# Kernel tuning notes

Measured on AMD Instinct MI355X. Metric: run time of the kernel, lower is better.

## Reference

```python
import jax, jax.numpy as jnp
import numpy as np

BETA = 0.95
SG_SLOPE = 25.0

@jax.custom_vjp
def spike(mem, thr):
    return (mem > thr).astype(mem.dtype)

def _spike_fwd(mem, thr):
    return spike(mem, thr), (mem, thr)

def _spike_bwd(res, g):
    mem, thr = res
    s = jax.nn.sigmoid(SG_SLOPE * (mem - thr))
    return (g * (SG_SLOPE * s * (1.0 - s)), jnp.zeros_like(thr))

spike.defvjp(_spike_fwd, _spike_bwd)

def setup_inputs() -> dict:
    key = jax.random.key(0)
    ks = jax.random.split(key, 7)
    T, B, IN, H, OUT = 50, 512, 784, 800, 10
    return {
        "x":  jax.random.normal(ks[0], (T, B, IN), dtype=jnp.float32),
        "W1": jax.random.normal(ks[1], (H, IN), dtype=jnp.float32) / np.sqrt(IN),
        "b1": jax.random.normal(ks[2], (H,), dtype=jnp.float32) * 0.01,
        "W2": jax.random.normal(ks[3], (H, H), dtype=jnp.float32) / np.sqrt(H),
        "b2": jax.random.normal(ks[4], (H,), dtype=jnp.float32) * 0.01,
        "W3": jax.random.normal(ks[5], (OUT, H), dtype=jnp.float32) / np.sqrt(H),
        "b3": jax.random.normal(ks[6], (OUT,), dtype=jnp.float32) * 0.01,
        "thresh1": jnp.ones((H,), dtype=jnp.float32),
        "thresh2": jnp.ones((H,), dtype=jnp.float32),
    }

def reference(x, W1, b1, W2, b2, W3, b3, thresh1, thresh2):
    T, B = x.shape[0], x.shape[1]
    H, OUT = W1.shape[0], W3.shape[0]
    # Batch the input projection across all timesteps: [T,B,H]
    x1 = jnp.einsum('tbi,hi->tbh', x, W1) + b1

    def step(carry, xt):
        mem1, mem2, mem3 = carry
        mem1 = BETA * mem1 + xt
        spk1 = spike(mem1, thresh1)
        mem1 = mem1 * (1.0 - spk1)
        mem2 = BETA * mem2 + spk1 @ W2.T + b2
        spk2 = spike(mem2, thresh2)
        mem2 = mem2 * (1.0 - spk2)
        mem3 = BETA * mem3 + spk2 @ W3.T + b3
        spk3 = spike(mem3, jnp.float32(1.0))
        mem3 = mem3 * (1.0 - spk3)
        return (mem1, mem2, mem3), (spk1, spk2, spk3)

    init = (jnp.zeros((B, H), x.dtype), jnp.zeros((B, H), x.dtype), jnp.zeros((B, OUT), x.dtype))
    _, (s1r, s2r, s3r) = jax.lax.scan(step, init, x1)
    return s3r.sum(0), s1r, s2r, s3r
```

## Files before the change

### kernel.cpp

```cpp
#include <hip/hip_runtime.h>

#define TT 50
#define BB 512
#define II 784
#define HH 800
#define OO 10
#define BH (BB*HH)
#define MM (TT*BB)

typedef double d4 __attribute__((ext_vector_type(4)));

__device__ __forceinline__ int dec16(double V) {
    const int vi = (int)(V + 0.5);
    const int a = vi - 96;
    if (a >= 0 && a < 64 && (a & 3) == 0) return a >> 2;
    return ((vi - 6) >> 4) & 15;
}
__device__ __forceinline__ bool isf1(double V) {
    const int vi = (int)(V + 0.5);
    const int a = vi - 96;
    return (a >= 0 && a < 64 && (a & 3) == 0);
}

__global__ __launch_bounds__(256) void k_gemm1(
    const float* __restrict__ x, const float* __restrict__ W1,
    const float* __restrict__ b1, double* __restrict__ x1d)
{
    __shared__ float As[16*144];
    __shared__ float Bs[16*80];
    const int m0 = blockIdx.x * 128;
    const int n0 = blockIdx.y * 80;
    const int tid = threadIdx.x;
    const int lane = tid & 63;
    const int wm = (tid >> 6) * 32;

    const d4 zc = {0.0, 0.0, 0.0, 0.0};
    const d4 pr = __builtin_amdgcn_mfma_f64_16x16x4f64(
        (double)lane, 1.0, zc, 0, 0, 0);
    const d4 pc = __builtin_amdgcn_mfma_f64_16x16x4f64(
        1.0, (double)lane, zc, 0, 0, 0);
    int rowIdx[4], colIdx[4];
    #pragma unroll
    for (int r = 0; r < 4; ++r) {
        rowIdx[r] = dec16(pr[r]) & 15;
        colIdx[r] = dec16(pc[r]) & 15;
    }
    const bool af1 = isf1(pr[0]);
    const bool bf1 = isf1(pc[0]);
    const int arow = af1 ? (lane & 15) : (lane >> 2);
    const int akk  = af1 ? (lane >> 4) : (lane & 3);
    const int bcol = bf1 ? (lane & 15) : (lane >> 2);
    const int bkk  = bf1 ? (lane >> 4) : (lane & 3);

    d4 acc[2][5] = {};

    const int sm = tid >> 1;
    const int sk = (tid & 1) * 8;
    const int bn0 = tid >> 2, bk0 = (tid & 3) * 4;
    const int q1  = tid + 256;
    const int bn1 = q1 >> 2,  bk1 = (q1 & 3) * 4;

    for (int k0 = 0; k0 < II; k0 += 16) {
        const float4 a0 = *(const float4*)(x + (long)(m0+sm)*II + k0 + sk);
        const float4 a1 = *(const float4*)(x + (long)(m0+sm)*II + k0 + sk + 4);
        const float4 w0 = *(const float4*)(W1 + (long)(n0+bn0)*II + k0 + bk0);
        float4 w1;
        if (tid < 64)
            w1 = *(const float4*)(W1 + (long)(n0+bn1)*II + k0 + bk1);
        __syncthreads();
        As[(sk+0)*144+sm] = a0.x;
        As[(sk+1)*144+sm] = a0.y;
        As[(sk+2)*144+sm] = a0.z;
        As[(sk+3)*144+sm] = a0.w;
        As[(sk+4)*144+sm] = a1.x;
        As[(sk+5)*144+sm] = a1.y;
        As[(sk+6)*144+sm] = a1.z;
        As[(sk+7)*144+sm] = a1.w;
        Bs[(bk0+0)*80+bn0] = w0.x;
        Bs[(bk0+1)*80+bn0] = w0.y;
        Bs[(bk0+2)*80+bn0] = w0.z;
        Bs[(bk0+3)*80+bn0] = w0.w;
        if (tid < 64) {
            Bs[(bk1+0)*80+bn1] = w1.x;
            Bs[(bk1+1)*80+bn1] = w1.y;
            Bs[(bk1+2)*80+bn1] = w1.z;
            Bs[(bk1+3)*80+bn1] = w1.w;
        }
        __syncthreads();
        #pragma unroll
        for (int s = 0; s < 4; ++s) {
            const int ka = 4*s + akk;
            const int kb = 4*s + bkk;
            const double a0d = (double)As[ka*144 + wm + arow];
            const double a1d = (double)As[ka*144 + wm + 16 + arow];
            double bd[5];
            #pragma unroll
            for (int j = 0; j < 5; ++j)
                bd[j] = (double)Bs[kb*80 + 16*j + bcol];
            #pragma unroll
            for (int j = 0; j < 5; ++j) {
                acc[0][j] = __builtin_amdgcn_mfma_f64_16x16x4f64(
                    a0d, bd[j], acc[0][j], 0, 0, 0);
                acc[1][j] = __builtin_amdgcn_mfma_f64_16x16x4f64(
                    a1d, bd[j], acc[1][j], 0, 0, 0);
            }
        }
    }
    #pragma unroll
    for (int i = 0; i < 2; ++i) {
        #pragma unroll
        for (int r = 0; r < 4; ++r) {
            const long m = m0 + wm + 16*i + rowIdx[r];
            #pragma unroll
            for (int j = 0; j < 5; ++j) {
                const int n = n0 + 16*j + colIdx[r];
                x1d[m*HH + n] = acc[i][j][r] + (double)b1[n];
            }
        }
    }
}

__global__ __launch_bounds__(256) void k_mem1(
    const double* __restrict__ x1d, const float* __restrict__ thresh1,
    unsigned char* __restrict__ s1c, float* __restrict__ s1r)
{
    const int lid = blockIdx.x*256 + threadIdx.x;
    const int h = lid % HH;
    const double th = (double)thresh1[h];
    double mem = 0.0;
    for (int t = 0; t < TT; ++t) {
        const long idx = (long)t*BH + lid;
        mem = 0.95*mem + x1d[idx];
        const bool spk = mem > th;
        s1c[idx] = spk ? 1 : 0;
        s1r[idx] = spk ? 1.0f : 0.0f;
        if (spk) mem = 0.0;
    }
}

__global__ __launch_bounds__(256) void k_gemm2(
    const unsigned char* __restrict__ s1c, const float* __restrict__ W2,
    float* __restrict__ z2)
{
    __shared__ float As[32*132];
    __shared__ float Bs[32*84];
    const int m0 = blockIdx.x * 128;
    const int n0 = blockIdx.y * 80;
    const int tid = threadIdx.x;
    const int tx = tid & 15, ty = tid >> 4;
    float acc[8][5] = {};

    const int sm = tid >> 1;
    const int sk = (tid & 1) * 16;
    const int b0n = tid >> 3,        b0k = (tid & 7) * 4;
    const int q1 = tid + 256, b1n = q1 >> 3, b1k = (q1 & 7) * 4;
    const int q2 = tid + 512, b2n = q2 >> 3, b2k = (q2 & 7) * 4;

    for (int k0 = 0; k0 < HH; k0 += 32) {
        const uint4 av = *(const uint4*)(s1c + (long)(m0+sm)*HH + k0 + sk);
        const float4 w0 = *(const float4*)(W2 + (long)(n0+b0n)*HH + k0 + b0k);
        const float4 w1 = *(const float4*)(W2 + (long)(n0+b1n)*HH + k0 + b1k);
        float4 w2;
        if (tid < 128)
            w2 = *(const float4*)(W2 + (long)(n0+b2n)*HH + k0 + b2k);
        __syncthreads();
        {
            const unsigned int d[4] = {av.x, av.y, av.z, av.w};
            #pragma unroll
            for (int w = 0; w < 4; ++w) {
                #pragma unroll
                for (int j = 0; j < 4; ++j)
                    As[(sk + w*4 + j)*132 + sm] =
                        (float)((d[w] >> (8*j)) & 0xffu);
            }
        }
        Bs[(b0k+0)*84+b0n] = w0.x; Bs[(b0k+1)*84+b0n] = w0.y;
        Bs[(b0k+2)*84+b0n] = w0.z; Bs[(b0k+3)*84+b0n] = w0.w;
        Bs[(b1k+0)*84+b1n] = w1.x; Bs[(b1k+1)*84+b1n] = w1.y;
        Bs[(b1k+2)*84+b1n] = w1.z; Bs[(b1k+3)*84+b1n] = w1.w;
        if (tid < 128) {
            Bs[(b2k+0)*84+b2n] = w2.x; Bs[(b2k+1)*84+b2n] = w2.y;
            Bs[(b2k+2)*84+b2n] = w2.z; Bs[(b2k+3)*84+b2n] = w2.w;
        }
        __syncthreads();
        #pragma unroll
        for (int k = 0; k < 32; ++k) {
            float a[8], b[5];
            #pragma unroll
            for (int i = 0; i < 8; ++i) a[i] = As[k*132 + ty*8 + i];
            #pragma unroll
            for (int j = 0; j < 4; ++j) b[j] = Bs[k*84 + tx*4 + j];
            b[4] = Bs[k*84 + 64 + tx];
            #pragma unroll
            for (int i = 0; i < 8; ++i)
                #pragma unroll
                for (int j = 0; j < 5; ++j)
                    acc[i][j] = __fmaf_rn(a[i], b[j], acc[i][j]);
        }
    }
    #pragma unroll
    for (int i = 0; i < 8; ++i) {
        const long m = m0 + ty*8 + i;
        #pragma unroll
        for (int j = 0; j < 4; ++j)
            z2[m*HH + n0 + tx*4 + j] = acc[i][j];
        z2[m*HH + n0 + 64 + tx] = acc[i][4];
    }
}

__global__ __launch_bounds__(256) void k_scan2(
    const float* __restrict__ z2, const float* __restrict__ b2,
    const float* __restrict__ thresh2, float* __restrict__ s2r,
    unsigned char* __restrict__ s2c)
{
    const int lid = blockIdx.x*256 + threadIdx.x;
    const int n = lid % HH;
    const float b2v = b2[n];
    const float thv = thresh2[n];
    float m = 0.0f;
    for (int t = 0; t < TT; ++t) {
        const long idx = (long)t*BH + lid;
        const float m2 = __fadd_rn(
            __fadd_rn(__fmul_rn(0.95f, m), z2[idx]), b2v);
        const bool spk = m2 > thv;
        s2r[idx] = spk ? 1.0f : 0.0f;
        s2c[idx] = spk ? 1 : 0;
        m = spk ? 0.0f : m2;
    }
}

__global__ __launch_bounds__(256) void k_gemm3(
    const unsigned char* __restrict__ s2c, const float* __restrict__ W3,
    float* __restrict__ z3)
{
    const long m = blockIdx.x*256 + threadIdx.x;
    const unsigned char* row = s2c + m*HH;
    float acc[10] = {};
    for (int k0 = 0; k0 < HH; k0 += 16) {
        const uint4 v = *(const uint4*)(row + k0);
        const unsigned int d[4] = {v.x, v.y, v.z, v.w};
        #pragma unroll
        for (int w = 0; w < 4; ++w) {
            #pragma unroll
            for (int j = 0; j < 4; ++j) {
                const float sv = (float)((d[w] >> (8*j)) & 0xffu);
                const int k = k0 + w*4 + j;
                #pragma unroll
                for (int o = 0; o < 10; ++o)
                    acc[o] = __fmaf_rn(sv, W3[o*HH + k], acc[o]);
            }
        }
    }
    #pragma unroll
    for (int o = 0; o < 10; ++o)
        z3[m*OO + o] = acc[o];
}

__global__ __launch_bounds__(256) void k_scan3(
    const float* __restrict__ z3, const float* __restrict__ b3,
    float* __restrict__ s3r, float* __restrict__ out0)
{
    const int gid = blockIdx.x*256 + threadIdx.x;
    if (gid >= BB*OO) return;
    const int o = gid % OO;
    const float b3v = b3[o];
    float mem = 0.0f, cnt = 0.0f;
    for (int t = 0; t < TT; ++t) {
        const float m3 = __fadd_rn(
            __fadd_rn(__fmul_rn(0.95f, mem), z3[(long)t*BB*OO + gid]), b3v);
        const bool spk = m3 > 1.0f;
        s3r[(long)t*BB*OO + gid] = spk ? 1.0f : 0.0f;
        if (spk) cnt = __fadd_rn(cnt, 1.0f);
        mem = spk ? 0.0f : m3;
    }
    out0[gid] = cnt;
}

extern "C" void kernel_launch(void* const* d_in, const int* in_sizes, int n_in,
                              void* d_out, int out_size, void* d_ws, size_t ws_size,
                              hipStream_t stream)
{
    const float* x   = (const float*)d_in[0];
    const float* W1  = (const float*)d_in[1];
    const float* b1  = (const float*)d_in[2];
    const float* W2  = (const float*)d_in[3];
    const float* b2  = (const float*)d_in[4];
    const float* W3  = (const float*)d_in[5];
    const float* b3  = (const float*)d_in[6];
    const float* th1 = (const float*)d_in[7];
    const float* th2 = (const float*)d_in[8];

    float* out0 = (float*)d_out;
    float* s1r  = out0 + BB*OO;
    float* s2r  = s1r + (long)TT*BH;
    float* s3r  = s2r + (long)TT*BH;

    char* p = (char*)d_ws;
    double* x1d = (double*)p;
    float*  z2  = (float*)p;
    float*  z3  = (float*)(p + 84000000);
    unsigned char* s1c = (unsigned char*)(p + 163840000);
    unsigned char* s2c = s1c + (size_t)TT*BH;
    (void)ws_size;

    k_gemm1<<<dim3(200,10), dim3(256), 0, stream>>>(x, W1, b1, x1d);
    k_mem1 <<<dim3(1600),   dim3(256), 0, stream>>>(x1d, th1, s1c, s1r);
    k_gemm2<<<dim3(200,10), dim3(256), 0, stream>>>(s1c, W2, z2);
    k_scan2<<<dim3(1600),   dim3(256), 0, stream>>>(z2, b2, th2, s2r, s2c);
    k_gemm3<<<dim3(100),    dim3(256), 0, stream>>>(s2c, W3, z3);
    k_scan3<<<dim3(20),     dim3(256), 0, stream>>>(z3, b3, s3r, out0);
}
```

Baseline: 1.406 ms.

## Double-buffer gemm1 shared tiles with register prefetch and deeper K chunks

Rewrites the input-projection GEMM main loop to use double-buffered shared memory with K chunks of 32 instead of 16. Global loads for chunk c+2 are issued into registers while chunk c is computed, and the store for chunk c+1 goes into the alternate buffer, so there is one barrier per chunk instead of two. This is meant to hide global memory latency and cut synchronisation. In exchange it roughly quadruples shared memory per block and raises register pressure, which could lower occupancy.

```diff
diff --git a/kernel.cpp b/kernel.cpp
--- a/kernel.cpp
+++ b/kernel.cpp
@@ -22,12 +22,37 @@
     return (a >= 0 && a < 64 && (a & 3) == 0);
 }
 
+template<int NS>
+__device__ __forceinline__ void gemm1_compute(
+    const float* __restrict__ Ab, const float* __restrict__ Bb,
+    int wm, int arow, int akk, int bcol, int bkk, d4 acc[2][5])
+{
+    #pragma unroll
+    for (int s = 0; s < NS; ++s) {
+        const int ka = 4*s + akk;
+        const int kb = 4*s + bkk;
+        const double a0d = (double)Ab[ka*144 + wm + arow];
+        const double a1d = (double)Ab[ka*144 + wm + 16 + arow];
+        double bd[5];
+        #pragma unroll
+        for (int j = 0; j < 5; ++j)
+            bd[j] = (double)Bb[kb*80 + 16*j + bcol];
+        #pragma unroll
+        for (int j = 0; j < 5; ++j) {
+            acc[0][j] = __builtin_amdgcn_mfma_f64_16x16x4f64(
+                a0d, bd[j], acc[0][j], 0, 0, 0);
+            acc[1][j] = __builtin_amdgcn_mfma_f64_16x16x4f64(
+                a1d, bd[j], acc[1][j], 0, 0, 0);
+        }
+    }
+}
+
 __global__ __launch_bounds__(256) void k_gemm1(
     const float* __restrict__ x, const float* __restrict__ W1,
     const float* __restrict__ b1, double* __restrict__ x1d)
 {
-    __shared__ float As[16*144];
-    __shared__ float Bs[16*80];
+    __shared__ float As[2][32*144];
+    __shared__ float Bs[2][32*80];
     const int m0 = blockIdx.x * 128;
     const int n0 = blockIdx.y * 80;
     const int tid = threadIdx.x;
@@ -54,58 +79,88 @@
 
     d4 acc[2][5] = {};
 
-    const int sm = tid >> 1;
-    const int sk = (tid & 1) * 8;
-    const int bn0 = tid >> 2, bk0 = (tid & 3) * 4;
-    const int q1  = tid + 256;
-    const int bn1 = q1 >> 2,  bk1 = (q1 & 3) * 4;
-
-    for (int k0 = 0; k0 < II; k0 += 16) {
-        const float4 a0 = *(const float4*)(x + (long)(m0+sm)*II + k0 + sk);
-        const float4 a1 = *(const float4*)(x + (long)(m0+sm)*II + k0 + sk + 4);
-        const float4 w0 = *(const float4*)(W1 + (long)(n0+bn0)*II + k0 + bk0);
-        float4 w1;
-        if (tid < 64)
-            w1 = *(const float4*)(W1 + (long)(n0+bn1)*II + k0 + bk1);
+    const int koff = (tid & 7) * 4;
+    const int r0   = tid >> 3;
+    const float* pA0 = x + (long)(m0 + r0      )*II + koff;
+    const float* pA1 = x + (long)(m0 + r0 + 32 )*II + koff;
+    const float* pA2 = x + (long)(m0 + r0 + 64 )*II + koff;
+    const float* pA3 = x + (long)(m0 + r0 + 96 )*II + koff;
+    const float* pB0 = W1 + (long)(n0 + r0     )*II + koff;
+    const float* pB1 = W1 + (long)(n0 + r0 + 32)*II + koff;
+    const int rB2 = (tid < 128) ? (r0 + 64) : 79;
+    const float* pB2 = W1 + (long)(n0 + rB2)*II + koff;
+
+    float4 RA0, RA1, RA2, RA3, RB0, RB1, RB2;
+
+#define G1_LOAD(c) do {                                                  \
+        const int _k0 = 32*(c);                                          \
+        const int _kc = ((c) == 24) ? 16 : 32;                           \
+        if (koff < _kc) {                                                \
+            RA0 = *(const float4*)(pA0 + _k0);                           \
+            RA1 = *(const float4*)(pA1 + _k0);                           \
+            RA2 = *(const float4*)(pA2 + _k0);                           \
+            RA3 = *(const float4*)(pA3 + _k0);                           \
+            RB0 = *(const float4*)(pB0 + _k0);                           \
+            RB1 = *(const float4*)(pB1 + _k0);                           \
+            if (tid < 128) RB2 = *(const float4*)(pB2 + _k0);            \
+        }                                                                \
+    } while (0)
+
+#define G1_STORE(c) do {                                                 \
+        float* _Ad = As[(c) & 1];                                        \
+        float* _Bd = Bs[(c) & 1];                                        \
+        const int _kc = ((c) == 24) ? 16 : 32;                           \
+        if (koff < _kc) {                                                \
+            _Ad[(koff+0)*144 + r0      ] = RA0.x;                        \
+            _Ad[(koff+1)*144 + r0      ] = RA0.y;                        \
+            _Ad[(koff+2)*144 + r0      ] = RA0.z;                        \
+            _Ad[(koff+3)*144 + r0      ] = RA0.w;                        \
+            _Ad[(koff+0)*144 + r0 + 32 ] = RA1.x;                        \
+            _Ad[(koff+1)*144 + r0 + 32 ] = RA1.y;                        \
+            _Ad[(koff+2)*144 + r0 + 32 ] = RA1.z;                        \
+            _Ad[(koff+3)*144 + r0 + 32 ] = RA1.w;                        \
+            _Ad[(koff+0)*144 + r0 + 64 ] = RA2.x;                        \
+            _Ad[(koff+1)*144 + r0 + 64 ] = RA2.y;                        \
+            _Ad[(koff+2)*144 + r0 + 64 ] = RA2.z;                        \
+            _Ad[(koff+3)*144 + r0 + 64 ] = RA2.w;                        \
+            _Ad[(koff+0)*144 + r0 + 96 ] = RA3.x;                        \
+            _Ad[(koff+1)*144 + r0 + 96 ] = RA3.y;                        \
+            _Ad[(koff+2)*144 + r0 + 96 ] = RA3.z;                        \
+            _Ad[(koff+3)*144 + r0 + 96 ] = RA3.w;                        \
+            _Bd[(koff+0)*80 + r0       ] = RB0.x;                        \
+            _Bd[(koff+1)*80 + r0       ] = RB0.y;                        \
+            _Bd[(koff+2)*80 + r0       ] = RB0.z;                        \
+            _Bd[(koff+3)*80 + r0       ] = RB0.w;                        \
+            _Bd[(koff+0)*80 + r0 + 32  ] = RB1.x;                        \
+            _Bd[(koff+1)*80 + r0 + 32  ] = RB1.y;                        \
+            _Bd[(koff+2)*80 + r0 + 32  ] = RB1.z;                        \
+            _Bd[(koff+3)*80 + r0 + 32  ] = RB1.w;                        \
+            if (tid < 128) {                                             \
+                _Bd[(koff+0)*80 + r0 + 64] = RB2.x;                      \
+                _Bd[(koff+1)*80 + r0 + 64] = RB2.y;                      \
+                _Bd[(koff+2)*80 + r0 + 64] = RB2.z;                      \
+                _Bd[(koff+3)*80 + r0 + 64] = RB2.w;                      \
+            }                                                            \
+        }                                                                \
+    } while (0)
+
+    G1_LOAD(0);
+    G1_STORE(0);
+    G1_LOAD(1);
+    __syncthreads();
+
+    for (int c = 0; c < 24; ++c) {
+        G1_STORE(c + 1);
+        if (c + 2 < 25) G1_LOAD(c + 2);
+        gemm1_compute<8>(As[c & 1], Bs[c & 1],
+                         wm, arow, akk, bcol, bkk, acc);
         __syncthreads();
-        As[(sk+0)*144+sm] = a0.x;
-        As[(sk+1)*144+sm] = a0.y;
-        As[(sk+2)*144+sm] = a0.z;
-        As[(sk+3)*144+sm] = a0.w;
-        As[(sk+4)*144+sm] = a1.x;
-        As[(sk+5)*144+sm] = a1.y;
-        As[(sk+6)*144+sm] = a1.z;
-        As[(sk+7)*144+sm] = a1.w;
-        Bs[(bk0+0)*80+bn0] = w0.x;
-        Bs[(bk0+1)*80+bn0] = w0.y;
-        Bs[(bk0+2)*80+bn0] = w0.z;
-        Bs[(bk0+3)*80+bn0] = w0.w;
-        if (tid < 64) {
-            Bs[(bk1+0)*80+bn1] = w1.x;
-            Bs[(bk1+1)*80+bn1] = w1.y;
-            Bs[(bk1+2)*80+bn1] = w1.z;
-            Bs[(bk1+3)*80+bn1] = w1.w;
-        }
-        __syncthreads();
-        #pragma unroll
-        for (int s = 0; s < 4; ++s) {
-            const int ka = 4*s + akk;
-            const int kb = 4*s + bkk;
-            const double a0d = (double)As[ka*144 + wm + arow];
-            const double a1d = (double)As[ka*144 + wm + 16 + arow];
-            double bd[5];
-            #pragma unroll
-            for (int j = 0; j < 5; ++j)
-                bd[j] = (double)Bs[kb*80 + 16*j + bcol];
-            #pragma unroll
-            for (int j = 0; j < 5; ++j) {
-                acc[0][j] = __builtin_amdgcn_mfma_f64_16x16x4f64(
-                    a0d, bd[j], acc[0][j], 0, 0, 0);
-                acc[1][j] = __builtin_amdgcn_mfma_f64_16x16x4f64(
-                    a1d, bd[j], acc[1][j], 0, 0, 0);
-            }
-        }
-    }
+    }
+    gemm1_compute<4>(As[0], Bs[0], wm, arow, akk, bcol, bkk, acc);
+
+#undef G1_LOAD
+#undef G1_STORE
+
     #pragma unroll
     for (int i = 0; i < 2; ++i) {
         #pragma unroll
```

New measurement: 1.523 ms. 1.08x slower.
